# Kernel optimization log

Hardware: AMD Instinct MI355X
Metric: run time of the kernel (lower is better)

## Reference

```python
import jax, jax.numpy as jnp
import numpy as np

N_EMBD = 1024
N_HEAD = 16
HEAD_DIM = N_EMBD // N_HEAD
BLOCK_SIZE = 2048
ROPE_BASE = 10000.0


def _rope_tables(dim, max_len, base=ROPE_BASE):
    half = dim // 2
    freqs = 1.0 / base ** (jnp.arange(half, dtype=jnp.float32) / half)
    angles = jnp.arange(max_len, dtype=jnp.float32)[:, None] * freqs[None, :]  # (T, half)
    return jnp.cos(angles), jnp.sin(angles)


def _apply_rope(x, cos, sin):
    # x: (B, H, T, D); cos/sin: (T, D//2)
    T = x.shape[2]
    c = cos[:T][None, None]
    s = sin[:T][None, None]
    x1 = x[..., ::2]
    x2 = x[..., 1::2]
    out = jnp.stack([x1 * c - x2 * s, x1 * s + x2 * c], axis=-1)  # (B,H,T,D//2,2)
    return out.reshape(x.shape)


def setup_inputs() -> dict:
    key = jax.random.key(0)
    k1, k2, k3, k4, k5 = jax.random.split(key, 5)
    B, T, C = 2, 2048, N_EMBD
    x = jax.random.normal(k1, (B, T, C), dtype=jnp.float32)
    scale = 1.0 / np.sqrt(C)
    Wqkv = jax.random.normal(k2, (C, 3 * C), dtype=jnp.float32) * scale
    bqkv = jax.random.normal(k3, (3 * C,), dtype=jnp.float32) * 0.01
    Wproj = jax.random.normal(k4, (C, C), dtype=jnp.float32) * scale
    bproj = jax.random.normal(k5, (C,), dtype=jnp.float32) * 0.01
    cos, sin = _rope_tables(HEAD_DIM, BLOCK_SIZE)
    return {"x": x, "Wqkv": Wqkv, "bqkv": bqkv, "Wproj": Wproj, "bproj": bproj,
            "cos": cos, "sin": sin}


def reference(x, Wqkv, bqkv, Wproj, bproj, cos, sin):
    B, T, C = x.shape
    H, D = N_HEAD, HEAD_DIM
    qkv = x @ Wqkv + bqkv  # (B,T,3C)
    q, k, v = jnp.split(qkv, 3, axis=-1)
    # (B,T,C) -> (B,H,T,D)
    q = q.reshape(B, T, H, D).transpose(0, 2, 1, 3)
    k = k.reshape(B, T, H, D).transpose(0, 2, 1, 3)
    v = v.reshape(B, T, H, D).transpose(0, 2, 1, 3)
    q = _apply_rope(q, cos, sin)
    k = _apply_rope(k, cos, sin)
    att = jnp.einsum('bhtd,bhsd->bhts', q, k) * (D ** -0.5)
    causal = jnp.tril(jnp.ones((T, T), dtype=bool))
    att = jnp.where(causal[None, None], att, -jnp.inf)
    att = jax.nn.softmax(att, axis=-1)
    y = jnp.einsum('bhts,bhsd->bhtd', att, v)  # (B,H,T,D)
    y = y.transpose(0, 2, 1, 3).reshape(B, T, C)
    return y @ Wproj + bproj
```

## Files before the change

kernel.cpp:

```cpp
#include <hip/hip_runtime.h>
#include <stdint.h>

typedef short s16x8 __attribute__((ext_vector_type(8)));
typedef float f32x4 __attribute__((ext_vector_type(4)));
typedef unsigned short u16;
typedef unsigned int u32;

__device__ __forceinline__ float bf2f(u16 u) {
  union { u32 i; float f; } v; v.i = ((u32)u) << 16; return v.f;
}
__device__ __forceinline__ u16 f2bf(float f) {
  union { float f; u32 i; } v; v.f = f;
  u32 i = v.i;
  return (u16)((i + 0x7fffu + ((i >> 16) & 1u)) >> 16);
}
__device__ __forceinline__ u16 f2bf_fast(float f) {
  union { float f; u32 i; } v; v.f = f;
  return (u16)((v.i + 0x8000u) >> 16);
}

__device__ __forceinline__ s16x8 load8(const void* p, size_t idx, int isf32) {
  s16x8 r;
  if (isf32) {
    const float* f = (const float*)p + idx;
    f32x4 a = *(const f32x4*)f;
    f32x4 b = *(const f32x4*)(f + 4);
#pragma unroll
    for (int j = 0; j < 4; j++) {
      r[j] = (short)f2bf(a[j]);
      r[4 + j] = (short)f2bf(b[j]);
    }
  } else {
    r = *(const s16x8*)((const u16*)p + idx);
  }
  return r;
}
__device__ __forceinline__ float loadf(const void* p, size_t idx, int isf32) {
  return isf32 ? ((const float*)p)[idx] : bf2f(((const u16*)p)[idx]);
}

__device__ __forceinline__ void cp16(const u16* g, u16* l) {
  __builtin_amdgcn_global_load_lds(
      (const __attribute__((address_space(1))) u32*)g,
      (__attribute__((address_space(3))) u32*)l, 16, 0, 0);
}

__global__ void detect_dtype(const u16* __restrict__ x, int* __restrict__ flags) {
  int cnt = 0;
  for (int i = threadIdx.x; i < 4096; i += 64) {
    int e = (x[i] >> 7) & 0xFF;
    if (e >= 0xF0) cnt++;
  }
  unsigned long long any = __ballot(cnt > 0);
  if (threadIdx.x == 0) {
    flags[0] = (any != 0ull) ? 1 : 0;
    flags[1] = 0;
  }
}

__global__ __launch_bounds__(256) void convert_x(const void* __restrict__ x,
                                                 const int* __restrict__ fp,
                                                 u16* __restrict__ xb) {
  size_t i = ((size_t)blockIdx.x * 256 + threadIdx.x) * 8;
  *(s16x8*)(xb + i) = load8(x, i, *fp);
}

__global__ __launch_bounds__(256) void transposeW2(
    const void* __restrict__ Wqkv, const void* __restrict__ Wproj,
    const int* __restrict__ fp, u16* __restrict__ WqkvT,
    u16* __restrict__ WprojT) {
  __shared__ u32 tile32[32 * 66];
  const int f = *fp;
  const int tid = threadIdx.x;
  const int bx = blockIdx.x;
  const void* W;
  u16* WT;
  int N, nb;
  if (bx < 48) { W = Wqkv; WT = WqkvT; N = 3072; nb = bx * 64; }
  else         { W = Wproj; WT = WprojT; N = 1024; nb = (bx - 48) * 64; }
  const int kb = blockIdx.y * 64;
  {
    int a = tid >> 3, c8 = tid & 7;
    s16x8 r0 = load8(W, (size_t)(kb + 2 * a) * N + nb + c8 * 8, f);
    s16x8 r1 = load8(W, (size_t)(kb + 2 * a + 1) * N + nb + c8 * 8, f);
#pragma unroll
    for (int j = 0; j < 8; j++)
      tile32[a * 66 + c8 * 8 + j] = (u32)(u16)r0[j] | ((u32)(u16)r1[j] << 16);
  }
  __syncthreads();
#pragma unroll
  for (int i = 0; i < 2; i++) {
    int idx = tid + i * 256;
    int n = idx >> 3, c8 = idx & 7;
    s16x8 v;
#pragma unroll
    for (int w = 0; w < 4; w++) {
      u32 pk = tile32[(c8 * 4 + w) * 66 + n];
      v[2 * w] = (short)(u16)(pk & 0xFFFF);
      v[2 * w + 1] = (short)(u16)(pk >> 16);
    }
    *(s16x8*)(WT + (size_t)(nb + n) * 1024 + kb + c8 * 8) = v;
  }
}

__global__ __launch_bounds__(256) void transposeV(const u16* __restrict__ qkv,
                                                  u16* __restrict__ vT) {
  __shared__ u32 tile32[64 * 33];
  const int tid = threadIdx.x;
  const int tb = blockIdx.x * 64, bh = blockIdx.y;
  const int b = bh >> 4, h = bh & 15;
  {
    int a = tid >> 3, c8 = tid & 7;
    const u16* base = qkv + (size_t)(b * 2048 + tb + 2 * a) * 3072 + 2048 + h * 64;
    s16x8 r0 = *(const s16x8*)(base + c8 * 8);
    s16x8 r1 = *(const s16x8*)(base + 3072 + c8 * 8);
#pragma unroll
    for (int j = 0; j < 8; j++)
      tile32[(c8 * 8 + j) * 33 + a] = (u32)(u16)r0[j] | ((u32)(u16)r1[j] << 16);
  }
  __syncthreads();
#pragma unroll
  for (int i = 0; i < 2; i++) {
    int idx = tid + i * 256;
    int d = idx >> 3, c8 = idx & 7;
    s16x8 v;
#pragma unroll
    for (int w = 0; w < 4; w++) {
      u32 pk = tile32[d * 33 + c8 * 4 + w];
      v[2 * w] = (short)(u16)(pk & 0xFFFF);
      v[2 * w + 1] = (short)(u16)(pk >> 16);
    }
    *(s16x8*)(vT + ((size_t)bh * 64 + d) * 2048 + tb + c8 * 8) = v;
  }
}

template <int NT>
__global__ __launch_bounds__(256) void gemm_bt(
    const u16* __restrict__ A, int lda, const u16* __restrict__ Bt,
    const void* __restrict__ bias, const int* __restrict__ fI32,
    void* __restrict__ C, int ropeMode, int outF,
    const void* __restrict__ cost, const void* __restrict__ sint, int N,
    int K) {
  constexpr int NTW = NT / 32;
  __shared__ __attribute__((aligned(16))) u16 As[128 * 32];
  __shared__ __attribute__((aligned(16))) u16 Bs[NT * 32];
  const int inf32 = *fI32;
  const int tid = threadIdx.x;
  const int wave = tid >> 6, lane = tid & 63, quad = lane >> 4, l16 = lane & 15;
  const int m0 = blockIdx.y * 128, n0 = blockIdx.x * NT;
  const int wm = (wave & 1) * 64, wn = (wave >> 1) * (NT / 2);
  const int lr = lane >> 2, lk = (lane & 3) * 8;
  f32x4 acc[4][NTW];
#pragma unroll
  for (int i = 0; i < 4; i++)
#pragma unroll
    for (int j = 0; j < NTW; j++) acc[i][j] = (f32x4){0.f, 0.f, 0.f, 0.f};

  const u16* aP = A + (size_t)(m0 + wave * 32 + lr) * lda + lk;
  const u16* bP = Bt + (size_t)(n0 + wave * (NT / 4) + lr) * K + lk;
  u16* asl = As + wave * 32 * 32;
  u16* bsl = Bs + wave * (NT / 4) * 32;

  for (int kb = 0; kb < K; kb += 32) {
    __syncthreads();
    cp16(aP + kb, asl);
    cp16(aP + kb + (size_t)16 * lda, asl + 16 * 32);
#pragma unroll
    for (int i = 0; i < NT / 64; i++)
      cp16(bP + kb + (size_t)(16 * i) * K, bsl + i * 16 * 32);
    __syncthreads();
    s16x8 af[4], bfr[NTW];
#pragma unroll
    for (int t = 0; t < 4; t++)
      af[t] = *(const s16x8*)(As + (wm + t * 16 + l16) * 32 + quad * 8);
#pragma unroll
    for (int t = 0; t < NTW; t++)
      bfr[t] = *(const s16x8*)(Bs + (wn + t * 16 + l16) * 32 + quad * 8);
#pragma unroll
    for (int mt = 0; mt < 4; mt++)
#pragma unroll
      for (int nt = 0; nt < NTW; nt++)
        acc[mt][nt] = __builtin_amdgcn_mfma_f32_16x16x32_bf16(
            af[mt], bfr[nt], acc[mt][nt], 0, 0, 0);
  }
#pragma unroll
  for (int nt = 0; nt < NTW; nt++) {
    int col = n0 + wn + nt * 16 + l16;
    float bv = loadf(bias, col, inf32);
    if (ropeMode && col < 2048) {
      int j = (col & 63) >> 1, odd = col & 1;
#pragma unroll
      for (int mt = 0; mt < 4; mt++)
#pragma unroll
        for (int r = 0; r < 4; r++) {
          int row = m0 + wm + mt * 16 + quad * 4 + r, t = row & 2047;
          float cv = loadf(cost, (size_t)t * 32 + j, inf32);
          float sv = loadf(sint, (size_t)t * 32 + j, inf32);
          float val = acc[mt][nt][r] + bv;
          float pr = __shfl_xor(val, 1);
          float res = odd ? (pr * sv + val * cv) : (val * cv - pr * sv);
          ((u16*)C)[(size_t)row * N + col] = f2bf(res);
        }
    } else if (outF && inf32) {
#pragma unroll
      for (int mt = 0; mt < 4; mt++)
#pragma unroll
        for (int r = 0; r < 4; r++) {
          int row = m0 + wm + mt * 16 + quad * 4 + r;
          ((float*)C)[(size_t)row * N + col] = acc[mt][nt][r] + bv;
        }
    } else {
#pragma unroll
      for (int mt = 0; mt < 4; mt++)
#pragma unroll
        for (int r = 0; r < 4; r++) {
          int row = m0 + wm + mt * 16 + quad * 4 + r;
          ((u16*)C)[(size_t)row * N + col] = f2bf(acc[mt][nt][r] + bv);
        }
    }
  }
}

__global__ __launch_bounds__(512) void attn_kernel(u16* qkv,
                                                   const u16* __restrict__ vT) {
  __shared__ __attribute__((aligned(16))) u16 Ks[64 * 72];
  __shared__ __attribute__((aligned(16))) u16 Vt[64 * 72];
  __shared__ __attribute__((aligned(16))) u16 Pl[8][16 * 72];
  const int tid = threadIdx.x;
  const int wave = tid >> 6, lane = tid & 63, quad = lane >> 4, l16 = lane & 15;
  const int cu = blockIdx.x & 255, round = blockIdx.x >> 8;
  const int p = cu >> 5, bh = cu & 31;
  const int qt = round ? p : 15 - p;
  const int h = bh & 15;
  const size_t rb = (size_t)(bh >> 4) * 2048;
  const int qb = qt * 128;
  const float SCALE = 0.18033688011112042f;

  s16x8 qa0, qa1;
  {
    const u16* qp = qkv + (rb + qb + wave * 16 + l16) * 3072 + h * 64;
    qa0 = *(const s16x8*)(qp + quad * 8);
    qa1 = *(const s16x8*)(qp + 32 + quad * 8);
  }

  f32x4 o[4];
  float l_r[4] = {0.f, 0.f, 0.f, 0.f};
#pragma unroll
  for (int i = 0; i < 4; i++) o[i] = (f32x4){0.f, 0.f, 0.f, 0.f};

  const int nchunks = 2 * qt + 2;
  const int srow = tid >> 3, sc8 = tid & 7;
  s16x8 kr, vr;
  {
    kr = *(const s16x8*)(qkv + (rb + srow) * 3072 + 1024 + h * 64 + sc8 * 8);
    vr = *(const s16x8*)(vT + ((size_t)bh * 64 + srow) * 2048 + sc8 * 8);
  }

  for (int c = 0; c < nchunks; c++) {
    const int sb = c * 64;
    __syncthreads();
    *(s16x8*)(Ks + srow * 72 + sc8 * 8) = kr;
    *(s16x8*)(Vt + srow * 72 + sc8 * 8) = vr;
    __syncthreads();
    if (c + 1 < nchunks) {
      const int nb = sb + 64;
      kr = *(const s16x8*)(qkv + (rb + nb + srow) * 3072 + 1024 + h * 64 +
                           sc8 * 8);
      vr = *(const s16x8*)(vT + ((size_t)bh * 64 + srow) * 2048 + nb + sc8 * 8);
    }

    if (sb > qb + wave * 16 + 15) continue;

    f32x4 S[4];
#pragma unroll
    for (int kf = 0; kf < 4; kf++) {
      s16x8 k0 = *(const s16x8*)(Ks + (kf * 16 + l16) * 72 + quad * 8);
      s16x8 k1 = *(const s16x8*)(Ks + (kf * 16 + l16) * 72 + 32 + quad * 8);
      f32x4 a = (f32x4){0.f, 0.f, 0.f, 0.f};
      a = __builtin_amdgcn_mfma_f32_16x16x32_bf16(qa0, k0, a, 0, 0, 0);
      a = __builtin_amdgcn_mfma_f32_16x16x32_bf16(qa1, k1, a, 0, 0, 0);
      S[kf] = a;
    }

    u16* P = Pl[wave];
    const int mq = qb + wave * 16;
    const bool needMask = (sb + 63) > mq;
#pragma unroll
    for (int r = 0; r < 4; r++) {
      const int qi = mq + quad * 4 + r;
#pragma unroll
      for (int kf = 0; kf < 4; kf++) {
        float pv = __builtin_amdgcn_exp2f(S[kf][r] * SCALE);
        if (needMask) pv = ((sb + kf * 16 + l16) <= qi) ? pv : 0.f;
        l_r[r] += pv;
        P[(quad * 4 + r) * 72 + kf * 16 + l16] = f2bf_fast(pv);
      }
    }
    asm volatile("s_waitcnt lgkmcnt(0)" ::: "memory");
    s16x8 pa0 = *(const s16x8*)(P + l16 * 72 + quad * 8);
    s16x8 pa1 = *(const s16x8*)(P + l16 * 72 + 32 + quad * 8);

#pragma unroll
    for (int dt = 0; dt < 4; dt++) {
      s16x8 vb0 = *(const s16x8*)(Vt + (dt * 16 + l16) * 72 + quad * 8);
      s16x8 vb1 = *(const s16x8*)(Vt + (dt * 16 + l16) * 72 + 32 + quad * 8);
      o[dt] = __builtin_amdgcn_mfma_f32_16x16x32_bf16(pa0, vb0, o[dt], 0, 0, 0);
      o[dt] = __builtin_amdgcn_mfma_f32_16x16x32_bf16(pa1, vb1, o[dt], 0, 0, 0);
    }
  }

  float inv[4];
#pragma unroll
  for (int r = 0; r < 4; r++) {
    float rs = l_r[r];
#pragma unroll
    for (int off = 8; off; off >>= 1) rs += __shfl_xor(rs, off);
    inv[r] = 1.0f / fmaxf(rs, 1e-30f);
  }
#pragma unroll
  for (int dt = 0; dt < 4; dt++)
#pragma unroll
    for (int r = 0; r < 4; r++)
      qkv[(rb + qb + wave * 16 + quad * 4 + r) * 3072 + 2048 + h * 64 +
          dt * 16 + l16] = f2bf(o[dt][r] * inv[r]);
}

extern "C" void kernel_launch(void* const* d_in, const int* in_sizes, int n_in,
                              void* d_out, int out_size, void* d_ws,
                              size_t ws_size, hipStream_t stream) {
  const void* x = d_in[0];
  const void* Wqkv = d_in[1];
  const void* bqkv = d_in[2];
  const void* Wproj = d_in[3];
  const void* bproj = d_in[4];
  const void* cost = d_in[5];
  const void* sint = d_in[6];

  int* flags = (int*)d_ws;
  u16* WqkvT = (u16*)d_ws + 128;
  u16* WprojT = WqkvT + (size_t)3072 * 1024;
  u16* qkv = WprojT + (size_t)1024 * 1024;
  u16* yb = qkv + 2048;
  u16* xb = (u16*)d_out;
  u16* vT = (u16*)d_out + (size_t)4096 * 1024;

  detect_dtype<<<1, 64, 0, stream>>>((const u16*)x, flags);
  convert_x<<<2048, 256, 0, stream>>>(x, flags, xb);
  transposeW2<<<dim3(64, 16), 256, 0, stream>>>(Wqkv, Wproj, flags, WqkvT,
                                                WprojT);
  gemm_bt<128><<<dim3(24, 32), 256, 0, stream>>>(
      xb, 1024, WqkvT, bqkv, flags, qkv, 1, 0, cost, sint, 3072, 1024);
  transposeV<<<dim3(32, 32), 256, 0, stream>>>(qkv, vT);
  attn_kernel<<<512, 512, 0, stream>>>(qkv, vT);
  gemm_bt<64><<<dim3(16, 32), 256, 0, stream>>>(
      yb, 3072, WprojT, bproj, flags, d_out, 0, 1, nullptr, nullptr, 1024,
      1024);
}
```

Before: 211.5 us.

## Move RoPE out of QKV GEMM epilogue and stage bf16 output via LDS

RoPE is removed from the QKV GEMM epilogue and applied instead in the V-transpose kernel, which now reads q/k rows in 16-byte vectors, rotates them in place, and loads cos/sin as vectors. The bf16 GEMM epilogue now writes accumulators into shared memory in two halves and then stores coalesced 16-byte rows to global memory, replacing scattered 2-byte stores. This is meant to cut uncoalesced stores and per-element table loads in the epilogue. In exchange it adds a read-modify-write pass over q/k and extra barriers in the epilogue.

```diff
diff --git a/kernel.cpp b/kernel.cpp
--- a/kernel.cpp
+++ b/kernel.cpp
@@ -43,6 +43,18 @@
   __builtin_amdgcn_global_load_lds(
       (const __attribute__((address_space(1))) u32*)g,
       (__attribute__((address_space(3))) u32*)l, 16, 0, 0);
+}
+
+__device__ __forceinline__ s16x8 rope8(s16x8 x, const float* c, const float* s) {
+  s16x8 out;
+#pragma unroll
+  for (int j = 0; j < 4; j++) {
+    float x1 = bf2f((u16)x[2 * j]);
+    float x2 = bf2f((u16)x[2 * j + 1]);
+    out[2 * j] = (short)f2bf(x1 * c[j] - x2 * s[j]);
+    out[2 * j + 1] = (short)f2bf(x1 * s[j] + x2 * c[j]);
+  }
+  return out;
 }
 
 __global__ void detect_dtype(const u16* __restrict__ x, int* __restrict__ flags) {
@@ -103,12 +115,17 @@
   }
 }
 
-__global__ __launch_bounds__(256) void transposeV(const u16* __restrict__ qkv,
-                                                  u16* __restrict__ vT) {
+__global__ __launch_bounds__(256) void postproc(u16* __restrict__ qkv,
+                                                u16* __restrict__ vT,
+                                                const void* __restrict__ cost,
+                                                const void* __restrict__ sint,
+                                                const int* __restrict__ fp) {
   __shared__ u32 tile32[64 * 33];
+  const int f = *fp;
   const int tid = threadIdx.x;
   const int tb = blockIdx.x * 64, bh = blockIdx.y;
   const int b = bh >> 4, h = bh & 15;
+
   {
     int a = tid >> 3, c8 = tid & 7;
     const u16* base = qkv + (size_t)(b * 2048 + tb + 2 * a) * 3072 + 2048 + h * 64;
@@ -118,6 +135,32 @@
     for (int j = 0; j < 8; j++)
       tile32[(c8 * 8 + j) * 33 + a] = (u32)(u16)r0[j] | ((u32)(u16)r1[j] << 16);
   }
+
+#pragma unroll
+  for (int g = 0; g < 2; g++) {
+    int gi = tid + g * 256;
+    int row = gi >> 3, c8 = gi & 7;
+    int t = tb + row;
+    size_t base = (size_t)(b * 2048 + t) * 3072 + h * 64 + c8 * 8;
+    float cc[4], ss[4];
+    if (f) {
+      f32x4 cv = *(const f32x4*)((const float*)cost + (size_t)t * 32 + c8 * 4);
+      f32x4 sv = *(const f32x4*)((const float*)sint + (size_t)t * 32 + c8 * 4);
+#pragma unroll
+      for (int k = 0; k < 4; k++) { cc[k] = cv[k]; ss[k] = sv[k]; }
+    } else {
+#pragma unroll
+      for (int k = 0; k < 4; k++) {
+        cc[k] = bf2f(((const u16*)cost)[(size_t)t * 32 + c8 * 4 + k]);
+        ss[k] = bf2f(((const u16*)sint)[(size_t)t * 32 + c8 * 4 + k]);
+      }
+    }
+    s16x8 q = *(const s16x8*)(qkv + base);
+    *(s16x8*)(qkv + base) = rope8(q, cc, ss);
+    s16x8 kk = *(const s16x8*)(qkv + base + 1024);
+    *(s16x8*)(qkv + base + 1024) = rope8(kk, cc, ss);
+  }
+
   __syncthreads();
 #pragma unroll
   for (int i = 0; i < 2; i++) {
@@ -138,12 +181,14 @@
 __global__ __launch_bounds__(256) void gemm_bt(
     const u16* __restrict__ A, int lda, const u16* __restrict__ Bt,
     const void* __restrict__ bias, const int* __restrict__ fI32,
-    void* __restrict__ C, int ropeMode, int outF,
-    const void* __restrict__ cost, const void* __restrict__ sint, int N,
-    int K) {
+    void* __restrict__ C, int outF, int N, int K) {
   constexpr int NTW = NT / 32;
-  __shared__ __attribute__((aligned(16))) u16 As[128 * 32];
-  __shared__ __attribute__((aligned(16))) u16 Bs[NT * 32];
+  constexpr int CS = NT + 4;
+  constexpr int STAGE = 128 * 32 + NT * 32;
+  constexpr int SMSZ = (STAGE > 64 * CS) ? STAGE : 64 * CS;
+  __shared__ __attribute__((aligned(16))) u16 SMEM[SMSZ];
+  u16* As = SMEM;
+  u16* Bs = SMEM + 128 * 32;
   const int inf32 = *fI32;
   const int tid = threadIdx.x;
   const int wave = tid >> 6, lane = tid & 63, quad = lane >> 4, l16 = lane & 15;
@@ -183,41 +228,49 @@
         acc[mt][nt] = __builtin_amdgcn_mfma_f32_16x16x32_bf16(
             af[mt], bfr[nt], acc[mt][nt], 0, 0, 0);
   }
-#pragma unroll
-  for (int nt = 0; nt < NTW; nt++) {
-    int col = n0 + wn + nt * 16 + l16;
-    float bv = loadf(bias, col, inf32);
-    if (ropeMode && col < 2048) {
-      int j = (col & 63) >> 1, odd = col & 1;
-#pragma unroll
-      for (int mt = 0; mt < 4; mt++)
-#pragma unroll
-        for (int r = 0; r < 4; r++) {
-          int row = m0 + wm + mt * 16 + quad * 4 + r, t = row & 2047;
-          float cv = loadf(cost, (size_t)t * 32 + j, inf32);
-          float sv = loadf(sint, (size_t)t * 32 + j, inf32);
-          float val = acc[mt][nt][r] + bv;
-          float pr = __shfl_xor(val, 1);
-          float res = odd ? (pr * sv + val * cv) : (val * cv - pr * sv);
-          ((u16*)C)[(size_t)row * N + col] = f2bf(res);
-        }
-    } else if (outF && inf32) {
+
+  float bv[NTW];
+#pragma unroll
+  for (int nt = 0; nt < NTW; nt++)
+    bv[nt] = loadf(bias, n0 + wn + nt * 16 + l16, inf32);
+
+  if (outF && inf32) {
+#pragma unroll
+    for (int nt = 0; nt < NTW; nt++) {
+      int col = n0 + wn + nt * 16 + l16;
 #pragma unroll
       for (int mt = 0; mt < 4; mt++)
 #pragma unroll
         for (int r = 0; r < 4; r++) {
           int row = m0 + wm + mt * 16 + quad * 4 + r;
-          ((float*)C)[(size_t)row * N + col] = acc[mt][nt][r] + bv;
+          ((float*)C)[(size_t)row * N + col] = acc[mt][nt][r] + bv[nt];
         }
-    } else {
+    }
+    return;
+  }
+
+  u16* Cs = SMEM;
+#pragma unroll
+  for (int half = 0; half < 2; half++) {
+    __syncthreads();
+    if ((wave & 1) == half) {
 #pragma unroll
       for (int mt = 0; mt < 4; mt++)
 #pragma unroll
-        for (int r = 0; r < 4; r++) {
-          int row = m0 + wm + mt * 16 + quad * 4 + r;
-          ((u16*)C)[(size_t)row * N + col] = f2bf(acc[mt][nt][r] + bv);
-        }
-    }
+        for (int nt = 0; nt < NTW; nt++)
+#pragma unroll
+          for (int r = 0; r < 4; r++)
+            Cs[(mt * 16 + quad * 4 + r) * CS + wn + nt * 16 + l16] =
+                f2bf(acc[mt][nt][r] + bv[nt]);
+    }
+    __syncthreads();
+    int row = tid >> 2, cg = tid & 3;
+    int colbase = cg * (NT / 4);
+    u16* gout = (u16*)C + (size_t)(m0 + half * 64 + row) * N + n0 + colbase;
+    const u16* lsrc = Cs + row * CS + colbase;
+#pragma unroll
+    for (int k2 = 0; k2 < NT / 32; k2++)
+      *(s16x8*)(gout + k2 * 8) = *(const s16x8*)(lsrc + k2 * 8);
   }
 }
 
@@ -348,11 +401,10 @@
   convert_x<<<2048, 256, 0, stream>>>(x, flags, xb);
   transposeW2<<<dim3(64, 16), 256, 0, stream>>>(Wqkv, Wproj, flags, WqkvT,
                                                 WprojT);
-  gemm_bt<128><<<dim3(24, 32), 256, 0, stream>>>(
-      xb, 1024, WqkvT, bqkv, flags, qkv, 1, 0, cost, sint, 3072, 1024);
-  transposeV<<<dim3(32, 32), 256, 0, stream>>>(qkv, vT);
+  gemm_bt<128><<<dim3(24, 32), 256, 0, stream>>>(xb, 1024, WqkvT, bqkv, flags,
+                                                 qkv, 0, 3072, 1024);
+  postproc<<<dim3(32, 32), 256, 0, stream>>>(qkv, vT, cost, sint, flags);
   attn_kernel<<<512, 512, 0, stream>>>(qkv, vT);
-  gemm_bt<64><<<dim3(16, 32), 256, 0, stream>>>(
-      yb, 3072, WprojT, bproj, flags, d_out, 0, 1, nullptr, nullptr, 1024,
-      1024);
-}
+  gemm_bt<64><<<dim3(16, 32), 256, 0, stream>>>(yb, 3072, WprojT, bproj, flags,
+                                                d_out, 1, 1024, 1024);
+}
```

Result: no change. 212.3 us (+0.4%).
